# Kernel optimization log

Measured on AMD Instinct MI355X. Metric: run time of the kernel, lower is better.

The kernel has to match this reference:

```python
import jax, jax.numpy as jnp
import numpy as np

E = 16           # num_experts
D = 4096         # hidden_size
F = 688          # per-expert SwiGLU intermediate size
N = 8192         # total tokens (bsz*seq_len)
CAP_FACTOR = 1.25


def setup_inputs() -> dict:
    key = jax.random.key(0)
    k1, k2, k3, k4, k5, k6 = jax.random.split(key, 6)
    return {
        "x": jax.random.normal(k1, (N, D), dtype=jnp.float32),
        "topk_idx": jax.random.randint(k2, (N,), 0, E, dtype=jnp.int32),
        "topk_scores": jax.random.uniform(k3, (N,), dtype=jnp.float32),
        "Wg": jax.random.normal(k4, (E, D, F), dtype=jnp.float32) * 0.02,
        "Wu": jax.random.normal(k5, (E, D, F), dtype=jnp.float32) * 0.02,
        "Wd": jax.random.normal(k6, (E, F, D), dtype=jnp.float32) * 0.02,
    }


def reference(x, topk_idx, topk_scores, Wg, Wu, Wd):
    # Switch-style top-1 MoE with capacity-based token dropping.
    # Deterministic variant: tokens beyond capacity are dropped in token order
    # (original uses randperm; the math pattern is identical).
    n, d = x.shape
    e = Wg.shape[0]
    cap = int(CAP_FACTOR * n / e)  # static under jit

    # position of each token within its assigned expert (0-based)
    oh = jax.nn.one_hot(topk_idx, e, dtype=jnp.int32)            # [N, E]
    pos = jnp.take_along_axis(jnp.cumsum(oh, axis=0) - 1,
                              topk_idx[:, None].astype(jnp.int32), axis=1)[:, 0]
    keep = pos < cap                                             # [N] bool

    # dispatch: scatter kept tokens into [E, cap, D]; dropped go to dummy row E
    e_safe = jnp.where(keep, topk_idx, e)
    p_safe = jnp.minimum(pos, cap - 1)
    buf = jnp.zeros((e + 1, cap, d), x.dtype).at[e_safe, p_safe].set(x)[:e]

    # per-expert SwiGLU FFN: down(silu(gate(x)) * up(x))
    h = jax.nn.silu(jnp.einsum('ecd,edf->ecf', buf, Wg)) \
        * jnp.einsum('ecd,edf->ecf', buf, Wu)                    # [E, cap, F]
    out = jnp.einsum('ecf,efd->ecd', h, Wd)                      # [E, cap, D]

    # combine: gather back, zero-pad dropped tokens, scale by gate scores
    y = out[topk_idx, p_safe] * keep[:, None].astype(x.dtype)
    y = y * topk_scores[:, None]
    return y
```

## Files before the change

### kernel.cpp

```cpp
#include <hip/hip_runtime.h>
#include <hip/hip_bf16.h>

#define E_ 16
#define D_ 4096
#define F_ 688
#define HS_ 704
#define N_ 8192
#define CAP_ 640

typedef __attribute__((ext_vector_type(8))) short bf16x8;
typedef __attribute__((ext_vector_type(4))) float f32x4;
typedef __attribute__((ext_vector_type(4))) float fvec4;
typedef __attribute__((ext_vector_type(8))) unsigned short usvec8;

__device__ __forceinline__ unsigned short f2bf(float f) {
    __hip_bfloat16 h = __float2bfloat16(f);
    return __builtin_bit_cast(unsigned short, h);
}
__device__ __forceinline__ int lidx(int row, int k) {
    return row * 64 + (((k >> 3) ^ (row & 7)) << 3) + (k & 7);
}

__global__ void k_dispatch(const int* __restrict__ idx,
                           int* __restrict__ slot_token,
                           int* __restrict__ row_of,
                           int* __restrict__ cnt) {
    __shared__ int hist[256][E_];
    const int t = threadIdx.x;
#pragma unroll
    for (int e = 0; e < E_; e++) hist[t][e] = 0;
    __syncthreads();
    const int base = t * (N_ / 256);
    for (int j = 0; j < N_ / 256; j++) {
        int e = idx[base + j];
        hist[t][e]++;
    }
    __syncthreads();
    if (t < E_) {
        int run = 0;
        for (int i = 0; i < 256; i++) { int v = hist[i][t]; hist[i][t] = run; run += v; }
        cnt[t] = run < CAP_ ? run : CAP_;
    }
    for (int s = t; s < E_ * CAP_; s += 256) slot_token[s] = -1;
    __syncthreads();
    for (int j = 0; j < N_ / 256; j++) {
        int i = base + j;
        int e = idx[i];
        int p = hist[t][e]++;
        if (p < CAP_) { slot_token[e * CAP_ + p] = i; row_of[i] = e * CAP_ + p; }
        else          { row_of[i] = -1; }
    }
}

__global__ void k_zero_dropped(const int* __restrict__ row_of, float* __restrict__ y) {
    const int i = blockIdx.x;
    if (row_of[i] >= 0) return;
    fvec4* yp = (fvec4*)(y + (size_t)i * D_);
    fvec4 z = {0.f, 0.f, 0.f, 0.f};
    for (int c = threadIdx.x; c < D_ / 4; c += 256) yp[c] = z;
}

__global__ void k_gather(const float* __restrict__ x, const int* __restrict__ slot_token,
                         unsigned short* __restrict__ Abuf) {
    const int slot = blockIdx.x;
    const int t = slot_token[slot];
    usvec8* dst = (usvec8*)(Abuf + (size_t)slot * D_);
    if (t < 0) {
        usvec8 z = {0, 0, 0, 0, 0, 0, 0, 0};
        for (int c = threadIdx.x; c < D_ / 8; c += 256) dst[c] = z;
    } else {
        const fvec4* src = (const fvec4*)(x + (size_t)t * D_);
        for (int c = threadIdx.x; c < D_ / 8; c += 256) {
            fvec4 a = src[2 * c], b = src[2 * c + 1];
            usvec8 p = {f2bf(a[0]), f2bf(a[1]), f2bf(a[2]), f2bf(a[3]),
                        f2bf(b[0]), f2bf(b[1]), f2bf(b[2]), f2bf(b[3])};
            dst[c] = p;
        }
    }
}

template <bool PRE>
__global__ __launch_bounds__(256, 4) void k_gemm1(
    const float* __restrict__ x, const unsigned short* __restrict__ Abuf,
    const float* __restrict__ Wg, const float* __restrict__ Wu,
    const int* __restrict__ slot_token, const int* __restrict__ cnt,
    unsigned short* __restrict__ H) {
    const int bid = blockIdx.x;
    const int xcd = bid & 7;
    const int j = bid >> 3;
    const int mb = j % 10;
    const int gl = j / 10;
    const int group = xcd * 22 + gl;
    const int e = group / 11, fidx = group % 11;
    const int m0 = mb * 64, f0 = fidx * 64;
    if (m0 >= cnt[e]) return;

    __shared__ __align__(16) unsigned short As[64 * 64];
    __shared__ __align__(16) unsigned short Bgs[64 * 64];
    __shared__ __align__(16) unsigned short Bus[64 * 64];
    __shared__ int tokS[64];

    const int tid = threadIdx.x;
    const int lane = tid & 63, wave = tid >> 6;
    const int wm = wave >> 1, wn = wave & 1;

    if (!PRE) {
        if (tid < 64) tokS[tid] = slot_token[e * CAP_ + m0 + tid];
        __syncthreads();
    }

    f32x4 accG[2][2], accU[2][2];
#pragma unroll
    for (int a = 0; a < 2; a++)
#pragma unroll
        for (int b = 0; b < 2; b++) {
            f32x4 z = {0.f, 0.f, 0.f, 0.f};
            accG[a][b] = z; accU[a][b] = z;
        }

    const int ar = tid >> 2, ak = (tid & 3) * 16;
    const int fpos = (tid & 31) * 2, kq8 = (tid >> 5) * 8;
    const int gf = f0 + fpos;
    const bool bvalid = gf < F_;
    const float2 fz2 = {0.f, 0.f};
    const float* WgE = Wg + (size_t)e * D_ * F_;
    const float* WuE = Wu + (size_t)e * D_ * F_;
    const unsigned short* Ae = Abuf + (size_t)(e * CAP_ + m0) * D_;

    for (int kc = 0; kc < D_; kc += 64) {
        if (PRE) {
#pragma unroll
            for (int s = 0; s < 2; s++)
                *(usvec8*)&As[lidx(ar, ak + s * 8)] =
                    *(const usvec8*)&Ae[(size_t)ar * D_ + kc + ak + s * 8];
        } else {
            int t = tokS[ar];
            const float* src = x + (size_t)(t < 0 ? 0 : t) * D_ + kc + ak;
            fvec4 v0 = {0.f,0.f,0.f,0.f}, v1 = v0, v2 = v0, v3 = v0;
            if (t >= 0) { v0 = *(const fvec4*)src;        v1 = *(const fvec4*)(src + 4);
                          v2 = *(const fvec4*)(src + 8);  v3 = *(const fvec4*)(src + 12); }
            usvec8 p0 = {f2bf(v0[0]), f2bf(v0[1]), f2bf(v0[2]), f2bf(v0[3]),
                         f2bf(v1[0]), f2bf(v1[1]), f2bf(v1[2]), f2bf(v1[3])};
            usvec8 p1 = {f2bf(v2[0]), f2bf(v2[1]), f2bf(v2[2]), f2bf(v2[3]),
                         f2bf(v3[0]), f2bf(v3[1]), f2bf(v3[2]), f2bf(v3[3])};
            *(usvec8*)&As[lidx(ar, ak)] = p0;
            *(usvec8*)&As[lidx(ar, ak + 8)] = p1;
        }
        {
            float2 g[8], u[8];
#pragma unroll
            for (int r = 0; r < 8; r++) {
                size_t off = (size_t)(kc + kq8 + r) * F_ + gf;
                g[r] = bvalid ? *(const float2*)(WgE + off) : fz2;
                u[r] = bvalid ? *(const float2*)(WuE + off) : fz2;
            }
            usvec8 pg0, pg1, pu0, pu1;
#pragma unroll
            for (int r = 0; r < 8; r++) {
                pg0[r] = (short)f2bf(g[r].x); pg1[r] = (short)f2bf(g[r].y);
                pu0[r] = (short)f2bf(u[r].x); pu1[r] = (short)f2bf(u[r].y);
            }
            *(usvec8*)&Bgs[lidx(fpos, kq8)]     = pg0;
            *(usvec8*)&Bgs[lidx(fpos + 1, kq8)] = pg1;
            *(usvec8*)&Bus[lidx(fpos, kq8)]     = pu0;
            *(usvec8*)&Bus[lidx(fpos + 1, kq8)] = pu1;
        }
        __syncthreads();
        __builtin_amdgcn_s_setprio(1);
#pragma unroll
        for (int kk = 0; kk < 64; kk += 32) {
            const int ko = kk + ((lane >> 4) << 3);
            bf16x8 av[2], bgv[2], buv[2];
#pragma unroll
            for (int mi = 0; mi < 2; mi++)
                av[mi] = *(const bf16x8*)&As[lidx(wm * 32 + mi * 16 + (lane & 15), ko)];
#pragma unroll
            for (int ni = 0; ni < 2; ni++) {
                int rr = wn * 32 + ni * 16 + (lane & 15);
                bgv[ni] = *(const bf16x8*)&Bgs[lidx(rr, ko)];
                buv[ni] = *(const bf16x8*)&Bus[lidx(rr, ko)];
            }
#pragma unroll
            for (int mi = 0; mi < 2; mi++)
#pragma unroll
                for (int ni = 0; ni < 2; ni++) {
                    accG[mi][ni] = __builtin_amdgcn_mfma_f32_16x16x32_bf16(av[mi], bgv[ni], accG[mi][ni], 0, 0, 0);
                    accU[mi][ni] = __builtin_amdgcn_mfma_f32_16x16x32_bf16(av[mi], buv[ni], accU[mi][ni], 0, 0, 0);
                }
        }
        __builtin_amdgcn_s_setprio(0);
        __syncthreads();
    }
#pragma unroll
    for (int mi = 0; mi < 2; mi++)
#pragma unroll
        for (int ni = 0; ni < 2; ni++) {
            int f = f0 + wn * 32 + ni * 16 + (lane & 15);
            if (f >= F_) continue;
            int rowb = m0 + wm * 32 + mi * 16 + ((lane >> 4) << 2);
#pragma unroll
            for (int q = 0; q < 4; q++) {
                float g = accG[mi][ni][q], u = accU[mi][ni][q];
                float h = g * u / (1.f + __expf(-g));
                H[(size_t)(e * CAP_ + rowb + q) * HS_ + f] = f2bf(h);
            }
        }
}

__global__ __launch_bounds__(256, 4) void k_gemm2(
    const unsigned short* __restrict__ H, const float* __restrict__ Wd,
    const int* __restrict__ slot_token, const int* __restrict__ cnt,
    const float* __restrict__ scores, float* __restrict__ y) {
    const int bid = blockIdx.x;
    const int xcd = bid & 7;
    const int j = bid >> 3;
    const int mb = j % 5;
    const int gl = j / 5;
    const int group = xcd * 128 + gl;
    const int e = group >> 6, didx = group & 63;
    const int m0 = mb * 128, d0 = didx * 64;
    if (m0 >= cnt[e]) return;

    __shared__ __align__(16) unsigned short As[128 * 64];
    __shared__ __align__(16) unsigned short Bts[64 * 64];
    __shared__ int tokS[128];
    __shared__ float scS[128];

    const int tid = threadIdx.x;
    const int lane = tid & 63, wave = tid >> 6;
    const int wm = wave >> 1, wn = wave & 1;

    if (tid < 128) {
        int t = slot_token[e * CAP_ + m0 + tid];
        tokS[tid] = t;
        scS[tid] = (t >= 0) ? scores[t] : 0.f;
    }
    __syncthreads();

    f32x4 acc[4][2];
#pragma unroll
    for (int a = 0; a < 4; a++)
#pragma unroll
        for (int b = 0; b < 2; b++) {
            f32x4 z = {0.f, 0.f, 0.f, 0.f};
            acc[a][b] = z;
        }

    const int ar = tid >> 1, ak = (tid & 1) * 32;
    const int dpos = (tid & 31) * 2, kq8 = (tid >> 5) * 8;
    const int gd = d0 + dpos;
    const float2 fz2 = {0.f, 0.f};
    const float* WdE = Wd + (size_t)e * F_ * D_;
    const unsigned short* He = H + (size_t)(e * CAP_ + m0) * HS_;

    for (int kc = 0; kc < 704; kc += 64) {
#pragma unroll
        for (int s = 0; s < 4; s++)
            *(usvec8*)&As[lidx(ar, ak + s * 8)] =
                *(const usvec8*)&He[(size_t)ar * HS_ + kc + ak + s * 8];
        {
            float2 b[8];
#pragma unroll
            for (int r = 0; r < 8; r++) {
                int kr = kc + kq8 + r;
                b[r] = (kr < F_) ? *(const float2*)(WdE + (size_t)kr * D_ + gd) : fz2;
            }
            usvec8 p0, p1;
#pragma unroll
            for (int r = 0; r < 8; r++) {
                p0[r] = (short)f2bf(b[r].x); p1[r] = (short)f2bf(b[r].y);
            }
            *(usvec8*)&Bts[lidx(dpos, kq8)]     = p0;
            *(usvec8*)&Bts[lidx(dpos + 1, kq8)] = p1;
        }
        __syncthreads();
        __builtin_amdgcn_s_setprio(1);
#pragma unroll
        for (int kk = 0; kk < 64; kk += 32) {
            const int ko = kk + ((lane >> 4) << 3);
            bf16x8 av[4], bv[2];
#pragma unroll
            for (int mi = 0; mi < 4; mi++)
                av[mi] = *(const bf16x8*)&As[lidx(wm * 64 + mi * 16 + (lane & 15), ko)];
#pragma unroll
            for (int ni = 0; ni < 2; ni++)
                bv[ni] = *(const bf16x8*)&Bts[lidx(wn * 32 + ni * 16 + (lane & 15), ko)];
#pragma unroll
            for (int mi = 0; mi < 4; mi++)
#pragma unroll
                for (int ni = 0; ni < 2; ni++)
                    acc[mi][ni] = __builtin_amdgcn_mfma_f32_16x16x32_bf16(av[mi], bv[ni], acc[mi][ni], 0, 0, 0);
        }
        __builtin_amdgcn_s_setprio(0);
        __syncthreads();
    }
#pragma unroll
    for (int mi = 0; mi < 4; mi++)
#pragma unroll
        for (int ni = 0; ni < 2; ni++) {
            int d = d0 + wn * 32 + ni * 16 + (lane & 15);
            int rowb = wm * 64 + mi * 16 + ((lane >> 4) << 2);
#pragma unroll
            for (int q = 0; q < 4; q++) {
                int row = rowb + q;
                int t = tokS[row];
                if (t >= 0) y[(size_t)t * D_ + d] = acc[mi][ni][q] * scS[row];
            }
        }
}

extern "C" void kernel_launch(void* const* d_in, const int* in_sizes, int n_in,
                              void* d_out, int out_size, void* d_ws, size_t ws_size,
                              hipStream_t stream) {
    const float* x   = (const float*)d_in[0];
    const int*   idx = (const int*)d_in[1];
    const float* sc  = (const float*)d_in[2];
    const float* Wg  = (const float*)d_in[3];
    const float* Wu  = (const float*)d_in[4];
    const float* Wd  = (const float*)d_in[5];
    float* y = (float*)d_out;

    char* ws = (char*)d_ws;
    int* slot_token = (int*)ws;
    int* row_of     = (int*)(ws + 40960);
    int* cnt        = (int*)(ws + 40960 + 32768);
    const size_t hoff = 131072;
    const size_t hbytes = (size_t)E_ * CAP_ * HS_ * 2;
    unsigned short* H = (unsigned short*)(ws + hoff);
    const size_t aoff = hoff + hbytes;
    const size_t abytes = (size_t)E_ * CAP_ * D_ * 2;
    unsigned short* Abuf = (unsigned short*)(ws + aoff);
    const bool pre = ws_size >= aoff + abytes;

    k_dispatch<<<1, 256, 0, stream>>>(idx, slot_token, row_of, cnt);
    k_zero_dropped<<<N_, 256, 0, stream>>>(row_of, y);
    if (pre) {
        k_gather<<<E_ * CAP_, 256, 0, stream>>>(x, slot_token, Abuf);
        k_gemm1<true><<<1760, 256, 0, stream>>>(x, Abuf, Wg, Wu, slot_token, cnt, H);
    } else {
        k_gemm1<false><<<1760, 256, 0, stream>>>(x, Abuf, Wg, Wu, slot_token, cnt, H);
    }
    k_gemm2<<<5120, 256, 0, stream>>>(H, Wd, slot_token, cnt, sc, y);
}
```

Before: 548.9 us.

## Pre-tile activations into swizzled LDS images and double-buffer both GEMMs with async loads

New measurement: 476.3 us. -13.2%, faster.

```diff
diff --git a/kernel.cpp b/kernel.cpp
--- a/kernel.cpp
+++ b/kernel.cpp
@@ -4,9 +4,10 @@
 #define E_ 16
 #define D_ 4096
 #define F_ 688
-#define HS_ 704
 #define N_ 8192
 #define CAP_ 640
+#define NKT_ 64
+#define NFT_ 11
 
 typedef __attribute__((ext_vector_type(8))) short bf16x8;
 typedef __attribute__((ext_vector_type(4))) float f32x4;
@@ -19,6 +20,14 @@
 }
 __device__ __forceinline__ int lidx(int row, int k) {
     return row * 64 + (((k >> 3) ^ (row & 7)) << 3) + (k & 7);
+}
+__device__ __forceinline__ int bidx(int row, int k) {
+    return row * 64 + (((k >> 3) ^ ((row >> 1) & 7)) << 3) + (k & 7);
+}
+__device__ __forceinline__ void gload16(const unsigned short* g, unsigned short* l) {
+    __builtin_amdgcn_global_load_lds(
+        (const __attribute__((address_space(1))) unsigned int*)g,
+        (__attribute__((address_space(3))) unsigned int*)l, 16, 0, 0);
 }
 
 __global__ void k_dispatch(const int* __restrict__ idx,
@@ -61,127 +70,138 @@
 }
 
 __global__ void k_gather(const float* __restrict__ x, const int* __restrict__ slot_token,
-                         unsigned short* __restrict__ Abuf) {
-    const int slot = blockIdx.x;
-    const int t = slot_token[slot];
-    usvec8* dst = (usvec8*)(Abuf + (size_t)slot * D_);
-    if (t < 0) {
-        usvec8 z = {0, 0, 0, 0, 0, 0, 0, 0};
-        for (int c = threadIdx.x; c < D_ / 8; c += 256) dst[c] = z;
-    } else {
-        const fvec4* src = (const fvec4*)(x + (size_t)t * D_);
-        for (int c = threadIdx.x; c < D_ / 8; c += 256) {
-            fvec4 a = src[2 * c], b = src[2 * c + 1];
-            usvec8 p = {f2bf(a[0]), f2bf(a[1]), f2bf(a[2]), f2bf(a[3]),
-                        f2bf(b[0]), f2bf(b[1]), f2bf(b[2]), f2bf(b[3])};
-            dst[c] = p;
-        }
-    }
-}
-
-template <bool PRE>
-__global__ __launch_bounds__(256, 4) void k_gemm1(
-    const float* __restrict__ x, const unsigned short* __restrict__ Abuf,
+                         unsigned short* __restrict__ Aimg) {
+    const int strip = blockIdx.y;
+    const int kg = blockIdx.x;
+    const int t = threadIdx.x;
+    const int r = t >> 1, h = t & 1;
+    const int tok = slot_token[strip * 128 + r];
+#pragma unroll
+    for (int kl4 = 0; kl4 < 4; kl4++) {
+        const int kt = kg * 4 + kl4;
+        const int k0 = kt * 64 + h * 32;
+        unsigned short* dst = Aimg + ((size_t)strip * NKT_ + kt) * 8192;
+        usvec8 p[4];
+        if (tok < 0) {
+            usvec8 z = {0, 0, 0, 0, 0, 0, 0, 0};
+            p[0] = z; p[1] = z; p[2] = z; p[3] = z;
+        } else {
+            const float* src = x + (size_t)tok * D_ + k0;
+#pragma unroll
+            for (int uu = 0; uu < 4; uu++) {
+                fvec4 a = *(const fvec4*)(src + uu * 8);
+                fvec4 b = *(const fvec4*)(src + uu * 8 + 4);
+                usvec8 q = {f2bf(a[0]), f2bf(a[1]), f2bf(a[2]), f2bf(a[3]),
+                            f2bf(b[0]), f2bf(b[1]), f2bf(b[2]), f2bf(b[3])};
+                p[uu] = q;
+            }
+        }
+#pragma unroll
+        for (int uu = 0; uu < 4; uu++)
+            *(usvec8*)&dst[lidx(r, h * 32 + uu * 8)] = p[uu];
+    }
+}
+
+__global__ __launch_bounds__(256, 2) void k_gemm1(
+    const unsigned short* __restrict__ Aimg,
     const float* __restrict__ Wg, const float* __restrict__ Wu,
-    const int* __restrict__ slot_token, const int* __restrict__ cnt,
-    unsigned short* __restrict__ H) {
+    const int* __restrict__ cnt, unsigned short* __restrict__ Himg) {
     const int bid = blockIdx.x;
     const int xcd = bid & 7;
     const int j = bid >> 3;
-    const int mb = j % 10;
-    const int gl = j / 10;
+    const int mb = j % 5;
+    const int gl = j / 5;
     const int group = xcd * 22 + gl;
-    const int e = group / 11, fidx = group % 11;
-    const int m0 = mb * 64, f0 = fidx * 64;
+    const int e = group / NFT_, fidx = group % NFT_;
+    const int m0 = mb * 128, f0 = fidx * 64;
     if (m0 >= cnt[e]) return;
-
-    __shared__ __align__(16) unsigned short As[64 * 64];
-    __shared__ __align__(16) unsigned short Bgs[64 * 64];
-    __shared__ __align__(16) unsigned short Bus[64 * 64];
-    __shared__ int tokS[64];
+    const int strip = e * 5 + mb;
+
+    __shared__ __align__(16) unsigned short As[2][128 * 64];
+    __shared__ __align__(16) unsigned short Bgs[2][64 * 64];
+    __shared__ __align__(16) unsigned short Bus[2][64 * 64];
 
     const int tid = threadIdx.x;
     const int lane = tid & 63, wave = tid >> 6;
     const int wm = wave >> 1, wn = wave & 1;
 
-    if (!PRE) {
-        if (tid < 64) tokS[tid] = slot_token[e * CAP_ + m0 + tid];
-        __syncthreads();
-    }
-
-    f32x4 accG[2][2], accU[2][2];
-#pragma unroll
-    for (int a = 0; a < 2; a++)
+    f32x4 accG[4][2], accU[4][2];
+#pragma unroll
+    for (int a = 0; a < 4; a++)
 #pragma unroll
         for (int b = 0; b < 2; b++) {
             f32x4 z = {0.f, 0.f, 0.f, 0.f};
             accG[a][b] = z; accU[a][b] = z;
         }
 
-    const int ar = tid >> 2, ak = (tid & 3) * 16;
     const int fpos = (tid & 31) * 2, kq8 = (tid >> 5) * 8;
     const int gf = f0 + fpos;
     const bool bvalid = gf < F_;
     const float2 fz2 = {0.f, 0.f};
     const float* WgE = Wg + (size_t)e * D_ * F_;
     const float* WuE = Wu + (size_t)e * D_ * F_;
-    const unsigned short* Ae = Abuf + (size_t)(e * CAP_ + m0) * D_;
-
-    for (int kc = 0; kc < D_; kc += 64) {
-        if (PRE) {
-#pragma unroll
-            for (int s = 0; s < 2; s++)
-                *(usvec8*)&As[lidx(ar, ak + s * 8)] =
-                    *(const usvec8*)&Ae[(size_t)ar * D_ + kc + ak + s * 8];
-        } else {
-            int t = tokS[ar];
-            const float* src = x + (size_t)(t < 0 ? 0 : t) * D_ + kc + ak;
-            fvec4 v0 = {0.f,0.f,0.f,0.f}, v1 = v0, v2 = v0, v3 = v0;
-            if (t >= 0) { v0 = *(const fvec4*)src;        v1 = *(const fvec4*)(src + 4);
-                          v2 = *(const fvec4*)(src + 8);  v3 = *(const fvec4*)(src + 12); }
-            usvec8 p0 = {f2bf(v0[0]), f2bf(v0[1]), f2bf(v0[2]), f2bf(v0[3]),
-                         f2bf(v1[0]), f2bf(v1[1]), f2bf(v1[2]), f2bf(v1[3])};
-            usvec8 p1 = {f2bf(v2[0]), f2bf(v2[1]), f2bf(v2[2]), f2bf(v2[3]),
-                         f2bf(v3[0]), f2bf(v3[1]), f2bf(v3[2]), f2bf(v3[3])};
-            *(usvec8*)&As[lidx(ar, ak)] = p0;
-            *(usvec8*)&As[lidx(ar, ak + 8)] = p1;
-        }
-        {
-            float2 g[8], u[8];
+    const unsigned short* Astrip = Aimg + (size_t)strip * NKT_ * 8192;
+
+    {
+#pragma unroll
+        for (int i = 0; i < 4; i++) {
+            int off = (wave * 4 + i) * 512;
+            gload16(Astrip + off + lane * 8, &As[0][off]);
+        }
+        float2 g[8], u[8];
+#pragma unroll
+        for (int r = 0; r < 8; r++) {
+            size_t off = (size_t)(kq8 + r) * F_ + gf;
+            g[r] = bvalid ? *(const float2*)(WgE + off) : fz2;
+            u[r] = bvalid ? *(const float2*)(WuE + off) : fz2;
+        }
+        usvec8 pg0, pg1, pu0, pu1;
+#pragma unroll
+        for (int r = 0; r < 8; r++) {
+            pg0[r] = (short)f2bf(g[r].x); pg1[r] = (short)f2bf(g[r].y);
+            pu0[r] = (short)f2bf(u[r].x); pu1[r] = (short)f2bf(u[r].y);
+        }
+        *(usvec8*)&Bgs[0][bidx(fpos, kq8)]     = pg0;
+        *(usvec8*)&Bgs[0][bidx(fpos + 1, kq8)] = pg1;
+        *(usvec8*)&Bus[0][bidx(fpos, kq8)]     = pu0;
+        *(usvec8*)&Bus[0][bidx(fpos + 1, kq8)] = pu1;
+    }
+    __syncthreads();
+
+    for (int kt = 0; kt < NKT_; ++kt) {
+        const int cur = kt & 1, nxt = cur ^ 1;
+        const bool hn = (kt + 1 < NKT_);
+        float2 g[8], u[8];
+        if (hn) {
+            const unsigned short* asrc = Astrip + (size_t)(kt + 1) * 8192;
+#pragma unroll
+            for (int i = 0; i < 4; i++) {
+                int off = (wave * 4 + i) * 512;
+                gload16(asrc + off + lane * 8, &As[nxt][off]);
+            }
 #pragma unroll
             for (int r = 0; r < 8; r++) {
-                size_t off = (size_t)(kc + kq8 + r) * F_ + gf;
+                size_t off = ((size_t)(kt + 1) * 64 + kq8 + r) * F_ + gf;
                 g[r] = bvalid ? *(const float2*)(WgE + off) : fz2;
                 u[r] = bvalid ? *(const float2*)(WuE + off) : fz2;
             }
-            usvec8 pg0, pg1, pu0, pu1;
-#pragma unroll
-            for (int r = 0; r < 8; r++) {
-                pg0[r] = (short)f2bf(g[r].x); pg1[r] = (short)f2bf(g[r].y);
-                pu0[r] = (short)f2bf(u[r].x); pu1[r] = (short)f2bf(u[r].y);
-            }
-            *(usvec8*)&Bgs[lidx(fpos, kq8)]     = pg0;
-            *(usvec8*)&Bgs[lidx(fpos + 1, kq8)] = pg1;
-            *(usvec8*)&Bus[lidx(fpos, kq8)]     = pu0;
-            *(usvec8*)&Bus[lidx(fpos + 1, kq8)] = pu1;
-        }
-        __syncthreads();
+        }
         __builtin_amdgcn_s_setprio(1);
 #pragma unroll
         for (int kk = 0; kk < 64; kk += 32) {
             const int ko = kk + ((lane >> 4) << 3);
-            bf16x8 av[2], bgv[2], buv[2];
-#pragma unroll
-            for (int mi = 0; mi < 2; mi++)
-                av[mi] = *(const bf16x8*)&As[lidx(wm * 32 + mi * 16 + (lane & 15), ko)];
+            bf16x8 av[4], bgv[2], buv[2];
+#pragma unroll
+            for (int mi = 0; mi < 4; mi++)
+                av[mi] = *(const bf16x8*)&As[cur][lidx(wm * 64 + mi * 16 + (lane & 15), ko)];
 #pragma unroll
             for (int ni = 0; ni < 2; ni++) {
                 int rr = wn * 32 + ni * 16 + (lane & 15);
-                bgv[ni] = *(const bf16x8*)&Bgs[lidx(rr, ko)];
-                buv[ni] = *(const bf16x8*)&Bus[lidx(rr, ko)];
-            }
-#pragma unroll
-            for (int mi = 0; mi < 2; mi++)
+                bgv[ni] = *(const bf16x8*)&Bgs[cur][bidx(rr, ko)];
+                buv[ni] = *(const bf16x8*)&Bus[cur][bidx(rr, ko)];
+            }
+#pragma unroll
+            for (int mi = 0; mi < 4; mi++)
 #pragma unroll
                 for (int ni = 0; ni < 2; ni++) {
                     accG[mi][ni] = __builtin_amdgcn_mfma_f32_16x16x32_bf16(av[mi], bgv[ni], accG[mi][ni], 0, 0, 0);
@@ -189,26 +209,39 @@
                 }
         }
         __builtin_amdgcn_s_setprio(0);
+        if (hn) {
+            usvec8 pg0, pg1, pu0, pu1;
+#pragma unroll
+            for (int r = 0; r < 8; r++) {
+                pg0[r] = (short)f2bf(g[r].x); pg1[r] = (short)f2bf(g[r].y);
+                pu0[r] = (short)f2bf(u[r].x); pu1[r] = (short)f2bf(u[r].y);
+            }
+            *(usvec8*)&Bgs[nxt][bidx(fpos, kq8)]     = pg0;
+            *(usvec8*)&Bgs[nxt][bidx(fpos + 1, kq8)] = pg1;
+            *(usvec8*)&Bus[nxt][bidx(fpos, kq8)]     = pu0;
+            *(usvec8*)&Bus[nxt][bidx(fpos + 1, kq8)] = pu1;
+        }
         __syncthreads();
     }
-#pragma unroll
-    for (int mi = 0; mi < 2; mi++)
+
+    unsigned short* Ht = Himg + ((size_t)strip * NFT_ + fidx) * 8192;
+#pragma unroll
+    for (int mi = 0; mi < 4; mi++)
 #pragma unroll
         for (int ni = 0; ni < 2; ni++) {
-            int f = f0 + wn * 32 + ni * 16 + (lane & 15);
-            if (f >= F_) continue;
-            int rowb = m0 + wm * 32 + mi * 16 + ((lane >> 4) << 2);
+            int fl = wn * 32 + ni * 16 + (lane & 15);
+            int rl = wm * 64 + mi * 16 + ((lane >> 4) << 2);
 #pragma unroll
             for (int q = 0; q < 4; q++) {
                 float g = accG[mi][ni][q], u = accU[mi][ni][q];
                 float h = g * u / (1.f + __expf(-g));
-                H[(size_t)(e * CAP_ + rowb + q) * HS_ + f] = f2bf(h);
-            }
-        }
-}
-
-__global__ __launch_bounds__(256, 4) void k_gemm2(
-    const unsigned short* __restrict__ H, const float* __restrict__ Wd,
+                Ht[lidx(rl + q, fl)] = f2bf(h);
+            }
+        }
+}
+
+__global__ __launch_bounds__(256, 3) void k_gemm2(
+    const unsigned short* __restrict__ Himg, const float* __restrict__ Wd,
     const int* __restrict__ slot_token, const int* __restrict__ cnt,
     const float* __restrict__ scores, float* __restrict__ y) {
     const int bid = blockIdx.x;
@@ -220,9 +253,10 @@
     const int e = group >> 6, didx = group & 63;
     const int m0 = mb * 128, d0 = didx * 64;
     if (m0 >= cnt[e]) return;
-
-    __shared__ __align__(16) unsigned short As[128 * 64];
-    __shared__ __align__(16) unsigned short Bts[64 * 64];
+    const int strip = e * 5 + mb;
+
+    __shared__ __align__(16) unsigned short As[2][128 * 64];
+    __shared__ __align__(16) unsigned short Bts[2][64 * 64];
     __shared__ int tokS[128];
     __shared__ float scS[128];
 
@@ -235,7 +269,6 @@
         tokS[tid] = t;
         scS[tid] = (t >= 0) ? scores[t] : 0.f;
     }
-    __syncthreads();
 
     f32x4 acc[4][2];
 #pragma unroll
@@ -246,34 +279,49 @@
             acc[a][b] = z;
         }
 
-    const int ar = tid >> 1, ak = (tid & 1) * 32;
     const int dpos = (tid & 31) * 2, kq8 = (tid >> 5) * 8;
     const int gd = d0 + dpos;
     const float2 fz2 = {0.f, 0.f};
     const float* WdE = Wd + (size_t)e * F_ * D_;
-    const unsigned short* He = H + (size_t)(e * CAP_ + m0) * HS_;
-
-    for (int kc = 0; kc < 704; kc += 64) {
-#pragma unroll
-        for (int s = 0; s < 4; s++)
-            *(usvec8*)&As[lidx(ar, ak + s * 8)] =
-                *(const usvec8*)&He[(size_t)ar * HS_ + kc + ak + s * 8];
-        {
-            float2 b[8];
+    const unsigned short* Hstrip = Himg + (size_t)strip * NFT_ * 8192;
+
+    {
+#pragma unroll
+        for (int i = 0; i < 4; i++) {
+            int off = (wave * 4 + i) * 512;
+            gload16(Hstrip + off + lane * 8, &As[0][off]);
+        }
+        float2 b[8];
+#pragma unroll
+        for (int r = 0; r < 8; r++) {
+            int kr = kq8 + r;
+            b[r] = (kr < F_) ? *(const float2*)(WdE + (size_t)kr * D_ + gd) : fz2;
+        }
+        usvec8 p0, p1;
+#pragma unroll
+        for (int r = 0; r < 8; r++) { p0[r] = (short)f2bf(b[r].x); p1[r] = (short)f2bf(b[r].y); }
+        *(usvec8*)&Bts[0][bidx(dpos, kq8)]     = p0;
+        *(usvec8*)&Bts[0][bidx(dpos + 1, kq8)] = p1;
+    }
+    __syncthreads();
+
+    for (int fc = 0; fc < NFT_; ++fc) {
+        const int cur = fc & 1, nxt = cur ^ 1;
+        const bool hn = (fc + 1 < NFT_);
+        float2 b[8];
+        if (hn) {
+            const unsigned short* asrc = Hstrip + (size_t)(fc + 1) * 8192;
+#pragma unroll
+            for (int i = 0; i < 4; i++) {
+                int off = (wave * 4 + i) * 512;
+                gload16(asrc + off + lane * 8, &As[nxt][off]);
+            }
 #pragma unroll
             for (int r = 0; r < 8; r++) {
-                int kr = kc + kq8 + r;
+                int kr = (fc + 1) * 64 + kq8 + r;
                 b[r] = (kr < F_) ? *(const float2*)(WdE + (size_t)kr * D_ + gd) : fz2;
             }
-            usvec8 p0, p1;
-#pragma unroll
-            for (int r = 0; r < 8; r++) {
-                p0[r] = (short)f2bf(b[r].x); p1[r] = (short)f2bf(b[r].y);
-            }
-            *(usvec8*)&Bts[lidx(dpos, kq8)]     = p0;
-            *(usvec8*)&Bts[lidx(dpos + 1, kq8)] = p1;
-        }
-        __syncthreads();
+        }
         __builtin_amdgcn_s_setprio(1);
 #pragma unroll
         for (int kk = 0; kk < 64; kk += 32) {
@@ -281,10 +329,10 @@
             bf16x8 av[4], bv[2];
 #pragma unroll
             for (int mi = 0; mi < 4; mi++)
-                av[mi] = *(const bf16x8*)&As[lidx(wm * 64 + mi * 16 + (lane & 15), ko)];
+                av[mi] = *(const bf16x8*)&As[cur][lidx(wm * 64 + mi * 16 + (lane & 15), ko)];
 #pragma unroll
             for (int ni = 0; ni < 2; ni++)
-                bv[ni] = *(const bf16x8*)&Bts[lidx(wn * 32 + ni * 16 + (lane & 15), ko)];
+                bv[ni] = *(const bf16x8*)&Bts[cur][bidx(wn * 32 + ni * 16 + (lane & 15), ko)];
 #pragma unroll
             for (int mi = 0; mi < 4; mi++)
 #pragma unroll
@@ -292,8 +340,16 @@
                     acc[mi][ni] = __builtin_amdgcn_mfma_f32_16x16x32_bf16(av[mi], bv[ni], acc[mi][ni], 0, 0, 0);
         }
         __builtin_amdgcn_s_setprio(0);
+        if (hn) {
+            usvec8 p0, p1;
+#pragma unroll
+            for (int r = 0; r < 8; r++) { p0[r] = (short)f2bf(b[r].x); p1[r] = (short)f2bf(b[r].y); }
+            *(usvec8*)&Bts[nxt][bidx(dpos, kq8)]     = p0;
+            *(usvec8*)&Bts[nxt][bidx(dpos + 1, kq8)] = p1;
+        }
         __syncthreads();
     }
+
 #pragma unroll
     for (int mi = 0; mi < 4; mi++)
 #pragma unroll
@@ -325,20 +381,14 @@
     int* row_of     = (int*)(ws + 40960);
     int* cnt        = (int*)(ws + 40960 + 32768);
     const size_t hoff = 131072;
-    const size_t hbytes = (size_t)E_ * CAP_ * HS_ * 2;
-    unsigned short* H = (unsigned short*)(ws + hoff);
+    const size_t hbytes = (size_t)80 * NFT_ * 8192 * 2;
+    unsigned short* Himg = (unsigned short*)(ws + hoff);
     const size_t aoff = hoff + hbytes;
-    const size_t abytes = (size_t)E_ * CAP_ * D_ * 2;
-    unsigned short* Abuf = (unsigned short*)(ws + aoff);
-    const bool pre = ws_size >= aoff + abytes;
+    unsigned short* Aimg = (unsigned short*)(ws + aoff);
 
     k_dispatch<<<1, 256, 0, stream>>>(idx, slot_token, row_of, cnt);
     k_zero_dropped<<<N_, 256, 0, stream>>>(row_of, y);
-    if (pre) {
-        k_gather<<<E_ * CAP_, 256, 0, stream>>>(x, slot_token, Abuf);
-        k_gemm1<true><<<1760, 256, 0, stream>>>(x, Abuf, Wg, Wu, slot_token, cnt, H);
-    } else {
-        k_gemm1<false><<<1760, 256, 0, stream>>>(x, Abuf, Wg, Wu, slot_token, cnt, H);
-    }
-    k_gemm2<<<5120, 256, 0, stream>>>(H, Wd, slot_token, cnt, sc, y);
-}
+    k_gather<<<dim3(16, 80), 256, 0, stream>>>(x, slot_token, Aimg);
+    k_gemm1<<<880, 256, 0, stream>>>(Aimg, Wg, Wu, cnt, Himg);
+    k_gemm2<<<5120, 256, 0, stream>>>(Himg, Wd, slot_token, cnt, sc, y);
+}
```
